# Performance work log

Measured on AMD Instinct MI355X. Metric: run time of the kernel, lower is better.

## Reference

```python
import jax, jax.numpy as jnp
import numpy as np

EPS = 1e-5

def layer_norm(x, w, b):
    m = jnp.mean(x, axis=-1, keepdims=True)
    v = jnp.mean(jnp.square(x - m), axis=-1, keepdims=True)
    return (x - m) * jax.lax.rsqrt(v + EPS) * w + b

def time_shift(x):
    # shift sequence right by one, zero-pad first step: (B,L,D)
    return jnp.pad(x[:, :-1], ((0, 0), (1, 0), (0, 0)))

def wkv(time_decay, time_first, k, v):
    # Numerically-stable RWKV v4 WKV recurrence. k,v: (B,L,D)
    w = -jnp.exp(time_decay)  # (D,) negative decay
    u = time_first            # (D,)
    B, L, D = k.shape
    kT = jnp.swapaxes(k, 0, 1)  # (L,B,D)
    vT = jnp.swapaxes(v, 0, 1)
    a0 = jnp.zeros((B, D), k.dtype)
    b0 = jnp.zeros((B, D), k.dtype)
    p0 = jnp.full((B, D), -1e38, k.dtype)

    def step(carry, kv_t):
        a, b, p = carry
        k_t, v_t = kv_t
        ww = u + k_t
        q = jnp.maximum(p, ww)
        e1 = jnp.exp(p - q)
        e2 = jnp.exp(ww - q)
        out = (e1 * a + e2 * v_t) / (e1 * b + e2)
        ww2 = p + w
        q2 = jnp.maximum(ww2, k_t)
        e1b = jnp.exp(ww2 - q2)
        e2b = jnp.exp(k_t - q2)
        return (e1b * a + e2b * v_t, e1b * b + e2b, q2), out

    _, outs = jax.lax.scan(step, (a0, b0, p0), (kT, vT))
    return jnp.swapaxes(outs, 0, 1)  # (B,L,D)

def setup_inputs() -> dict:
    key = jax.random.key(0)
    B, L, D, D_att, D_ffn = 8, 2048, 1024, 1024, 4096
    ks = jax.random.split(key, 16)
    s = 1.0 / np.sqrt(D)
    inp = {
        "x": jax.random.normal(ks[0], (B, L, D), jnp.float32),
        "ln_att_w": jnp.ones((D,), jnp.float32),
        "ln_att_b": jnp.zeros((D,), jnp.float32),
        "ln_ffn_w": jnp.ones((D,), jnp.float32),
        "ln_ffn_b": jnp.zeros((D,), jnp.float32),
        "att_time_decay": jax.random.normal(ks[1], (D_att,), jnp.float32) * 0.5,
        "att_time_first": jax.random.normal(ks[2], (D_att,), jnp.float32) * 0.5,
        "att_mix_k": jax.random.uniform(ks[3], (D,), jnp.float32),
        "att_mix_v": jax.random.uniform(ks[4], (D,), jnp.float32),
        "att_mix_r": jax.random.uniform(ks[5], (D,), jnp.float32),
        "att_Wk": jax.random.normal(ks[6], (D_att, D), jnp.float32) * s,
        "att_Wv": jax.random.normal(ks[7], (D_att, D), jnp.float32) * s,
        "att_Wr": jax.random.normal(ks[8], (D_att, D), jnp.float32) * s,
        "att_Wo": jax.random.normal(ks[9], (D, D_att), jnp.float32) * s,
        "ffn_mix_k": jax.random.uniform(ks[10], (D,), jnp.float32),
        "ffn_mix_r": jax.random.uniform(ks[11], (D,), jnp.float32),
        "ffn_Wk": jax.random.normal(ks[12], (D_ffn, D), jnp.float32) * s,
        "ffn_Wv": jax.random.normal(ks[13], (D, D_ffn), jnp.float32) * (1.0 / np.sqrt(D_ffn)),
        "ffn_Wr": jax.random.normal(ks[14], (D, D), jnp.float32) * s,
    }
    return inp

def rwkv_block(x, ln_att_w, ln_att_b, ln_ffn_w, ln_ffn_b,
               att_time_decay, att_time_first, att_mix_k, att_mix_v, att_mix_r,
               att_Wk, att_Wv, att_Wr, att_Wo,
               ffn_mix_k, ffn_mix_r, ffn_Wk, ffn_Wv, ffn_Wr):
    # --- time-mix (WKV attention) ---
    xa = layer_norm(x, ln_att_w, ln_att_b)
    xs = time_shift(xa)
    k = jnp.einsum('bld,ad->bla', xa * att_mix_k + xs * (1.0 - att_mix_k), att_Wk)
    v = jnp.einsum('bld,ad->bla', xa * att_mix_v + xs * (1.0 - att_mix_v), att_Wv)
    r = jnp.einsum('bld,ad->bla', xa * att_mix_r + xs * (1.0 - att_mix_r), att_Wr)
    att = jnp.einsum('bla,da->bld', jax.nn.sigmoid(r) * wkv(att_time_decay, att_time_first, k, v), att_Wo)
    x = x + att
    # --- channel-mix FFN ---
    xf = layer_norm(x, ln_ffn_w, ln_ffn_b)
    xs = time_shift(xf)
    kx = xf * ffn_mix_k + xs * (1.0 - ffn_mix_k)
    rx = xf * ffn_mix_r + xs * (1.0 - ffn_mix_r)
    h = jnp.square(jax.nn.relu(jnp.einsum('bld,fd->blf', kx, ffn_Wk)))
    ffn = jax.nn.sigmoid(jnp.einsum('bld,ed->ble', rx, ffn_Wr)) * jnp.einsum('blf,df->bld', h, ffn_Wv)
    return x + ffn

def reference(x, ln_att_w, ln_att_b, ln_ffn_w, ln_ffn_b,
              att_time_decay, att_time_first, att_mix_k, att_mix_v, att_mix_r,
              att_Wk, att_Wv, att_Wr, att_Wo,
              ffn_mix_k, ffn_mix_r, ffn_Wk, ffn_Wv, ffn_Wr):
    return rwkv_block(x, ln_att_w, ln_att_b, ln_ffn_w, ln_ffn_b,
                      att_time_decay, att_time_first, att_mix_k, att_mix_v, att_mix_r,
                      att_Wk, att_Wv, att_Wr, att_Wo,
                      ffn_mix_k, ffn_mix_r, ffn_Wk, ffn_Wv, ffn_Wr)
```

## Files before the change

### kernel.cpp

```cpp
#include <hip/hip_runtime.h>
#include <stdint.h>

#define DDIM 1024
#define LSEQ 2048
#define BSZ  8
#define FDIM 4096
#define MROWS (BSZ*LSEQ)
#define NCHUNK 32
#define CLEN  (LSEQ/NCHUNK)

typedef float        f32x4  __attribute__((ext_vector_type(4)));
typedef unsigned int u32x4  __attribute__((ext_vector_type(4)));

using gas_void = const __attribute__((address_space(1))) void;
using las_void = __attribute__((address_space(3))) void;

__device__ __forceinline__ void gload16(const void* g, void* l) {
    __builtin_amdgcn_global_load_lds((gas_void*)g, (las_void*)l, 16, 0, 0);
}

__device__ __forceinline__ void mfma_bf16(f32x4& d, u32x4 a, u32x4 b) {
    asm("v_mfma_f32_16x16x32_bf16 %0, %1, %2, %0" : "+v"(d) : "v"(a), "v"(b));
}

__device__ __forceinline__ unsigned short f2bf(float f) {
    __bf16 h = (__bf16)f;
    return __builtin_bit_cast(unsigned short, h);
}

__global__ __launch_bounds__(256) void cvt_bf16(const float* __restrict__ src,
                                                __bf16* __restrict__ dst, int n4)
{
    int i = blockIdx.x * 256 + threadIdx.x;
    if (i >= n4) return;
    float4 f = ((const float4*)src)[i];
    ushort4 o;
    o.x = f2bf(f.x); o.y = f2bf(f.y); o.z = f2bf(f.z); o.w = f2bf(f.w);
    ((ushort4*)dst)[i] = o;
}

__device__ __forceinline__ void blk_reduce4(float& a, float& b, float& c, float& d) {
#pragma unroll
    for (int off = 32; off >= 1; off >>= 1) {
        a += __shfl_xor(a, off, 64);
        b += __shfl_xor(b, off, 64);
        c += __shfl_xor(c, off, 64);
        d += __shfl_xor(d, off, 64);
    }
    __shared__ float sm[4][4];
    const int tid = threadIdx.x;
    if ((tid & 63) == 0) {
        sm[tid >> 6][0] = a; sm[tid >> 6][1] = b;
        sm[tid >> 6][2] = c; sm[tid >> 6][3] = d;
    }
    __syncthreads();
    a = sm[0][0] + sm[1][0] + sm[2][0] + sm[3][0];
    b = sm[0][1] + sm[1][1] + sm[2][1] + sm[3][1];
    c = sm[0][2] + sm[1][2] + sm[2][2] + sm[3][2];
    d = sm[0][3] + sm[1][3] + sm[2][3] + sm[3][3];
}

__global__ __launch_bounds__(256) void ln_mix3(
    const float* __restrict__ xin, const float* __restrict__ lnw, const float* __restrict__ lnb,
    const float* __restrict__ mkv, const float* __restrict__ mvv, const float* __restrict__ mrv,
    __bf16* __restrict__ ok, __bf16* __restrict__ ov, __bf16* __restrict__ orr)
{
    const int row = blockIdx.x;
    const int l   = row & (LSEQ - 1);
    const int tid = threadIdx.x;
    const size_t rbase = (size_t)row * DDIM;
    const float4 cur = ((const float4*)(xin + rbase))[tid];
    float4 prv = make_float4(0.f, 0.f, 0.f, 0.f);
    if (l > 0) prv = ((const float4*)(xin + rbase - DDIM))[tid];
    float s0 = cur.x + cur.y + cur.z + cur.w;
    float q0 = cur.x*cur.x + cur.y*cur.y + cur.z*cur.z + cur.w*cur.w;
    float s1 = prv.x + prv.y + prv.z + prv.w;
    float q1 = prv.x*prv.x + prv.y*prv.y + prv.z*prv.z + prv.w*prv.w;
    blk_reduce4(s0, q0, s1, q1);
    const float inv = 1.f / (float)DDIM;
    const float m0 = s0 * inv, m1 = s1 * inv;
    const float r0 = rsqrtf(fmaxf(q0 * inv - m0*m0, 0.f) + 1e-5f);
    const float r1 = rsqrtf(fmaxf(q1 * inv - m1*m1, 0.f) + 1e-5f);
    const float4 w4 = ((const float4*)lnw)[tid];
    const float4 b4 = ((const float4*)lnb)[tid];
    const float4 k4 = ((const float4*)mkv)[tid];
    const float4 v4 = ((const float4*)mvv)[tid];
    const float4 r4 = ((const float4*)mrv)[tid];
    const float cA[4] = {cur.x, cur.y, cur.z, cur.w};
    const float pA[4] = {prv.x, prv.y, prv.z, prv.w};
    const float wA[4] = {w4.x, w4.y, w4.z, w4.w};
    const float bA[4] = {b4.x, b4.y, b4.z, b4.w};
    const float kA[4] = {k4.x, k4.y, k4.z, k4.w};
    const float vA[4] = {v4.x, v4.y, v4.z, v4.w};
    const float rA[4] = {r4.x, r4.y, r4.z, r4.w};
    ushort4 pk, pv, pr;
    unsigned short* pkp = &pk.x; unsigned short* pvp = &pv.x; unsigned short* prp = &pr.x;
#pragma unroll
    for (int j = 0; j < 4; ++j) {
        float xa = (cA[j] - m0) * r0 * wA[j] + bA[j];
        float xs = (l > 0) ? ((pA[j] - m1) * r1 * wA[j] + bA[j]) : 0.f;
        pkp[j] = f2bf(xa * kA[j] + xs * (1.f - kA[j]));
        pvp[j] = f2bf(xa * vA[j] + xs * (1.f - vA[j]));
        prp[j] = f2bf(xa * rA[j] + xs * (1.f - rA[j]));
    }
    const size_t oi = (size_t)row * (DDIM/4) + tid;
    ((ushort4*)ok)[oi]  = pk;
    ((ushort4*)ov)[oi]  = pv;
    ((ushort4*)orr)[oi] = pr;
}

__global__ __launch_bounds__(256) void ln_mix2(
    const float* __restrict__ xin, const float* __restrict__ lnw, const float* __restrict__ lnb,
    const float* __restrict__ mkv, const float* __restrict__ mrv,
    __bf16* __restrict__ ok, __bf16* __restrict__ orr)
{
    const int row = blockIdx.x;
    const int l   = row & (LSEQ - 1);
    const int tid = threadIdx.x;
    const size_t rbase = (size_t)row * DDIM;
    const float4 cur = ((const float4*)(xin + rbase))[tid];
    float4 prv = make_float4(0.f, 0.f, 0.f, 0.f);
    if (l > 0) prv = ((const float4*)(xin + rbase - DDIM))[tid];
    float s0 = cur.x + cur.y + cur.z + cur.w;
    float q0 = cur.x*cur.x + cur.y*cur.y + cur.z*cur.z + cur.w*cur.w;
    float s1 = prv.x + prv.y + prv.z + prv.w;
    float q1 = prv.x*prv.x + prv.y*prv.y + prv.z*prv.z + prv.w*prv.w;
    blk_reduce4(s0, q0, s1, q1);
    const float inv = 1.f / (float)DDIM;
    const float m0 = s0 * inv, m1 = s1 * inv;
    const float r0 = rsqrtf(fmaxf(q0 * inv - m0*m0, 0.f) + 1e-5f);
    const float r1 = rsqrtf(fmaxf(q1 * inv - m1*m1, 0.f) + 1e-5f);
    const float4 w4 = ((const float4*)lnw)[tid];
    const float4 b4 = ((const float4*)lnb)[tid];
    const float4 k4 = ((const float4*)mkv)[tid];
    const float4 r4 = ((const float4*)mrv)[tid];
    const float cA[4] = {cur.x, cur.y, cur.z, cur.w};
    const float pA[4] = {prv.x, prv.y, prv.z, prv.w};
    const float wA[4] = {w4.x, w4.y, w4.z, w4.w};
    const float bA[4] = {b4.x, b4.y, b4.z, b4.w};
    const float kA[4] = {k4.x, k4.y, k4.z, k4.w};
    const float rA[4] = {r4.x, r4.y, r4.z, r4.w};
    ushort4 pk, pr;
    unsigned short* pkp = &pk.x; unsigned short* prp = &pr.x;
#pragma unroll
    for (int j = 0; j < 4; ++j) {
        float xa = (cA[j] - m0) * r0 * wA[j] + bA[j];
        float xs = (l > 0) ? ((pA[j] - m1) * r1 * wA[j] + bA[j]) : 0.f;
        pkp[j] = f2bf(xa * kA[j] + xs * (1.f - kA[j]));
        prp[j] = f2bf(xa * rA[j] + xs * (1.f - rA[j]));
    }
    const size_t oi = (size_t)row * (DDIM/4) + tid;
    ((ushort4*)ok)[oi]  = pk;
    ((ushort4*)orr)[oi] = pr;
}


__global__ __launch_bounds__(256) void wkv_phase1(
    const __bf16* __restrict__ kin, const __bf16* __restrict__ vin,
    const float* __restrict__ td,
    float* __restrict__ sa, float* __restrict__ sb, float* __restrict__ sp)
{
    const int idx = blockIdx.x * 256 + threadIdx.x;
    const int d  = idx & (DDIM - 1);
    const int bc = idx >> 10;
    const int b  = bc & (BSZ - 1);
    const int c  = bc >> 3;
    const float w = -__expf(td[d]);
    const size_t base = ((size_t)b * LSEQ + (size_t)c * CLEN) * DDIM + d;
    float a = 0.f, bbv = 0.f, p = -1e38f;
    for (int t = 0; t < CLEN; ++t) {
        const size_t off = base + (size_t)t * DDIM;
        const float kt = (float)kin[off];
        const float vt = (float)vin[off];
        const float ww2 = p + w;
        const float q2  = fmaxf(ww2, kt);
        const float e1  = __expf(ww2 - q2);
        const float e2  = __expf(kt - q2);
        a   = e1 * a   + e2 * vt;
        bbv = e1 * bbv + e2;
        p   = q2;
    }
    sa[idx] = a; sb[idx] = bbv; sp[idx] = p;
}

__global__ __launch_bounds__(256) void wkv_phase2(
    const __bf16* __restrict__ kin, const __bf16* __restrict__ vin,
    const __bf16* __restrict__ srin,
    const float* __restrict__ td, const float* __restrict__ tf,
    const float* __restrict__ sa, const float* __restrict__ sb,
    const float* __restrict__ sp,
    __bf16* __restrict__ outp)
{
    const int idx = blockIdx.x * 256 + threadIdx.x;
    const int d  = idx & (DDIM - 1);
    const int bc = idx >> 10;
    const int b  = bc & (BSZ - 1);
    const int c  = bc >> 3;
    const float w = -__expf(td[d]);
    const float u = tf[d];
    const float nw = (float)CLEN * w;

    float a = 0.f, bbv = 0.f, p = -1e38f;
    for (int j = 0; j < c; ++j) {
        const int sidx = ((j * BSZ + b) << 10) + d;
        const float aj = sa[sidx], bj = sb[sidx], pj = sp[sidx];
        const float ps = p + nw;
        const float pn = fmaxf(ps, pj);
        const float e1 = __expf(ps - pn);
        const float e2 = __expf(pj - pn);
        a   = e1 * a   + e2 * aj;
        bbv = e1 * bbv + e2 * bj;
        p   = pn;
    }

    const size_t base = ((size_t)b * LSEQ + (size_t)c * CLEN) * DDIM + d;
    for (int t = 0; t < CLEN; ++t) {
        const size_t off = base + (size_t)t * DDIM;
        const float kt = (float)kin[off];
        const float vt = (float)vin[off];
        const float sr = (float)srin[off];
        const float ww = u + kt;
        const float q  = fmaxf(p, ww);
        const float e1 = __expf(p - q);
        const float e2 = __expf(ww - q);
        const float o  = (e1 * a + e2 * vt) / (e1 * bbv + e2);
        outp[off] = (__bf16)(sr * o);
        const float ww2 = p + w;
        const float q2  = fmaxf(ww2, kt);
        const float e1b = __expf(ww2 - q2);
        const float e2b = __expf(kt - q2);
        a   = e1b * a   + e2b * vt;
        bbv = e1b * bbv + e2b;
        p   = q2;
    }
}

template<int EPI>
__global__ __launch_bounds__(256)
void gemm_bt(const __bf16* __restrict__ A, const __bf16* __restrict__ Bw,
             float* outF, __bf16* outH,
             const float* auxF, const __bf16* __restrict__ auxH,
             int N, int K)
{
    __shared__ __bf16 As[128 * 32];
    __shared__ __bf16 Bs[128 * 32];
    const int tid  = threadIdx.x;
    const int lane = tid & 63;
    const int wid  = tid >> 6;
    const int wr = wid >> 1, wc = wid & 1;
    const size_t row0 = (size_t)blockIdx.x * 128;
    const size_t col0 = (size_t)blockIdx.y * 128;

    const int c0 = wid * 2, c1 = c0 + 1;
    const int srow = lane >> 2;
    const int scol = (lane & 3) << 3;
    const __bf16* aG0 = A  + (row0 + c0 * 16 + srow) * (size_t)K + scol;
    const __bf16* aG1 = A  + (row0 + c1 * 16 + srow) * (size_t)K + scol;
    const __bf16* bG0 = Bw + (col0 + c0 * 16 + srow) * (size_t)K + scol;
    const __bf16* bG1 = Bw + (col0 + c1 * 16 + srow) * (size_t)K + scol;
    __bf16* aL0 = &As[c0 * 512];
    __bf16* aL1 = &As[c1 * 512];
    __bf16* bL0 = &Bs[c0 * 512];
    __bf16* bL1 = &Bs[c1 * 512];

    f32x4 acc[4][4] = {};

    const int aoff = (wr * 64 + (lane & 15)) * 32 + ((lane >> 4) << 3);
    const int boff = (wc * 64 + (lane & 15)) * 32 + ((lane >> 4) << 3);

    for (int k0 = 0; k0 < K; k0 += 32) {
        __syncthreads();
        gload16(aG0 + k0, aL0);
        gload16(aG1 + k0, aL1);
        gload16(bG0 + k0, bL0);
        gload16(bG1 + k0, bL1);
        __syncthreads();
        u32x4 af[4], bf[4];
#pragma unroll
        for (int m = 0; m < 4; ++m) af[m] = *(const u32x4*)&As[aoff + m * 512];
#pragma unroll
        for (int n = 0; n < 4; ++n) bf[n] = *(const u32x4*)&Bs[boff + n * 512];
#pragma unroll
        for (int m = 0; m < 4; ++m)
#pragma unroll
            for (int n = 0; n < 4; ++n)
                mfma_bf16(acc[m][n], af[m], bf[n]);
    }
    asm volatile("s_nop 7\n\ts_nop 7\n\ts_nop 3");

    const size_t obr = row0 + wr * 64 + ((lane >> 4) << 2);
    const size_t obc = col0 + wc * 64 + (lane & 15);
#pragma unroll
    for (int m = 0; m < 4; ++m) {
#pragma unroll
        for (int n = 0; n < 4; ++n) {
#pragma unroll
            for (int j = 0; j < 4; ++j) {
                const size_t idx = (obr + m * 16 + j) * (size_t)N + obc + n * 16;
                const float v = acc[m][n][j];
                if constexpr (EPI == 1) {
                    outH[idx] = (__bf16)(1.f / (1.f + __expf(-v)));
                } else if constexpr (EPI == 2) {
                    const float t = fmaxf(v, 0.f);
                    outH[idx] = (__bf16)(t * t);
                } else if constexpr (EPI == 3) {
                    outF[idx] = auxF[idx] + v;
                } else if constexpr (EPI == 4) {
                    outF[idx] = auxF[idx] + (float)auxH[idx] * v;
                } else {
                    outH[idx] = (__bf16)v;
                }
            }
        }
    }
}

extern "C" void kernel_launch(void* const* d_in, const int* in_sizes, int n_in,
                              void* d_out, int out_size, void* d_ws, size_t ws_size,
                              hipStream_t stream)
{
    const float* x    = (const float*)d_in[0];
    const float* lnaw = (const float*)d_in[1];
    const float* lnab = (const float*)d_in[2];
    const float* lnfw = (const float*)d_in[3];
    const float* lnfb = (const float*)d_in[4];
    const float* tdec = (const float*)d_in[5];
    const float* tfir = (const float*)d_in[6];
    const float* amk  = (const float*)d_in[7];
    const float* amv  = (const float*)d_in[8];
    const float* amr  = (const float*)d_in[9];
    const float* aWk  = (const float*)d_in[10];
    const float* aWv  = (const float*)d_in[11];
    const float* aWr  = (const float*)d_in[12];
    const float* aWo  = (const float*)d_in[13];
    const float* fmk  = (const float*)d_in[14];
    const float* fmr  = (const float*)d_in[15];
    const float* fWk  = (const float*)d_in[16];
    const float* fWv  = (const float*)d_in[17];
    const float* fWr  = (const float*)d_in[18];
    float* out = (float*)d_out;

    char* ws = (char*)d_ws;
    const size_t MiB = 1ull << 20;
    __bf16* Wk_h  = (__bf16*)ws;
    __bf16* Wv_h  = Wk_h + (1ull << 20);
    __bf16* Wr_h  = Wk_h + (2ull << 20);
    __bf16* Wo_h  = Wk_h + (3ull << 20);
    __bf16* fWk_h = Wk_h + (4ull << 20);
    __bf16* fWv_h = Wk_h + (8ull << 20);
    __bf16* fWr_h = Wk_h + (12ull << 20);
    __bf16* xk = (__bf16*)(ws + 26 * MiB);
    __bf16* xv = (__bf16*)(ws + 58 * MiB);
    __bf16* xr = (__bf16*)(ws + 90 * MiB);
    __bf16* kb = (__bf16*)(ws + 122 * MiB);
    __bf16* vb = (__bf16*)(ws + 154 * MiB);
    __bf16* sr = (__bf16*)(ws + 186 * MiB);
    float* st_a = (float*)(ws + 218 * MiB);
    float* st_b = (float*)(ws + 219 * MiB);
    float* st_p = (float*)(ws + 220 * MiB);
    __bf16* atta = xk;
    __bf16* kx   = xv;
    __bf16* rx   = xr;
    __bf16* sb   = xk;
    __bf16* hb   = (__bf16*)(ws + 90 * MiB);

    cvt_bf16<<<1024, 256, 0, stream>>>(aWk, Wk_h,  1 << 18);
    cvt_bf16<<<1024, 256, 0, stream>>>(aWv, Wv_h,  1 << 18);
    cvt_bf16<<<1024, 256, 0, stream>>>(aWr, Wr_h,  1 << 18);
    cvt_bf16<<<1024, 256, 0, stream>>>(aWo, Wo_h,  1 << 18);
    cvt_bf16<<<4096, 256, 0, stream>>>(fWk, fWk_h, 1 << 20);
    cvt_bf16<<<4096, 256, 0, stream>>>(fWv, fWv_h, 1 << 20);
    cvt_bf16<<<1024, 256, 0, stream>>>(fWr, fWr_h, 1 << 18);

    ln_mix3<<<MROWS, 256, 0, stream>>>(x, lnaw, lnab, amk, amv, amr, xk, xv, xr);

    dim3 blk(256);
    dim3 gD(MROWS / 128, DDIM / 128);
    gemm_bt<5><<<gD, blk, 0, stream>>>(xk, Wk_h, nullptr, kb, nullptr, nullptr, DDIM, DDIM);
    gemm_bt<5><<<gD, blk, 0, stream>>>(xv, Wv_h, nullptr, vb, nullptr, nullptr, DDIM, DDIM);
    gemm_bt<1><<<gD, blk, 0, stream>>>(xr, Wr_h, nullptr, sr, nullptr, nullptr, DDIM, DDIM);

    const int nthreads = BSZ * DDIM * NCHUNK;
    wkv_phase1<<<nthreads / 256, 256, 0, stream>>>(kb, vb, tdec, st_a, st_b, st_p);
    wkv_phase2<<<nthreads / 256, 256, 0, stream>>>(kb, vb, sr, tdec, tfir,
                                                   st_a, st_b, st_p, atta);

    gemm_bt<3><<<gD, blk, 0, stream>>>(atta, Wo_h, out, nullptr, x, nullptr, DDIM, DDIM);

    ln_mix2<<<MROWS, 256, 0, stream>>>(out, lnfw, lnfb, fmk, fmr, kx, rx);

    gemm_bt<1><<<gD, blk, 0, stream>>>(rx, fWr_h, nullptr, sb, nullptr, nullptr, DDIM, DDIM);

    dim3 gF(MROWS / 128, FDIM / 128);
    gemm_bt<2><<<gF, blk, 0, stream>>>(kx, fWk_h, nullptr, hb, nullptr, nullptr, FDIM, DDIM);

    gemm_bt<4><<<gD, blk, 0, stream>>>(hb, fWv_h, out, nullptr, out, sb, DDIM, FDIM);
}
```

Measured before the change: 796.3 us.

## Replace GEMM with 256x256-tile, 8-wave, multi-buffered swizzled-LDS kernel

Replaces the 128x128 single-buffered bf16 MFMA GEMM with a 256x256-tile kernel using 512 threads, a 4-deep LDS ring with XOR-swizzled layout, and prefetch two k-steps ahead using vmcnt waits. Adds an XCD-aware block remapping and s_setprio around MFMA bursts. The aim is more data reuse per tile, fewer LDS bank conflicts, and hiding global load latency behind compute. In exchange it uses 128 KB of shared memory and many accumulator registers, which may limit occupancy.

```diff
diff --git a/kernel.cpp b/kernel.cpp
--- a/kernel.cpp
+++ b/kernel.cpp
@@ -154,7 +154,6 @@
     ((ushort4*)orr)[oi] = pr;
 }
 
-
 __global__ __launch_bounds__(256) void wkv_phase1(
     const __bf16* __restrict__ kin, const __bf16* __restrict__ vin,
     const float* __restrict__ td,
@@ -236,62 +235,94 @@
 }
 
 template<int EPI>
-__global__ __launch_bounds__(256)
-void gemm_bt(const __bf16* __restrict__ A, const __bf16* __restrict__ Bw,
-             float* outF, __bf16* outH,
-             const float* auxF, const __bf16* __restrict__ auxH,
-             int N, int K)
-{
-    __shared__ __bf16 As[128 * 32];
-    __shared__ __bf16 Bs[128 * 32];
+__global__ __launch_bounds__(512, 2)
+void gemm8(const __bf16* __restrict__ A, const __bf16* __restrict__ Bw,
+           float* outF, __bf16* outH,
+           const float* auxF, const __bf16* __restrict__ auxH,
+           int N, int K, int gy)
+{
+    __shared__ __align__(16) char smem[131072];
     const int tid  = threadIdx.x;
     const int lane = tid & 63;
     const int wid  = tid >> 6;
-    const int wr = wid >> 1, wc = wid & 1;
-    const size_t row0 = (size_t)blockIdx.x * 128;
-    const size_t col0 = (size_t)blockIdx.y * 128;
-
-    const int c0 = wid * 2, c1 = c0 + 1;
-    const int srow = lane >> 2;
-    const int scol = (lane & 3) << 3;
-    const __bf16* aG0 = A  + (row0 + c0 * 16 + srow) * (size_t)K + scol;
-    const __bf16* aG1 = A  + (row0 + c1 * 16 + srow) * (size_t)K + scol;
-    const __bf16* bG0 = Bw + (col0 + c0 * 16 + srow) * (size_t)K + scol;
-    const __bf16* bG1 = Bw + (col0 + c1 * 16 + srow) * (size_t)K + scol;
-    __bf16* aL0 = &As[c0 * 512];
-    __bf16* aL1 = &As[c1 * 512];
-    __bf16* bL0 = &Bs[c0 * 512];
-    __bf16* bL1 = &Bs[c1 * 512];
-
-    f32x4 acc[4][4] = {};
-
-    const int aoff = (wr * 64 + (lane & 15)) * 32 + ((lane >> 4) << 3);
-    const int boff = (wc * 64 + (lane & 15)) * 32 + ((lane >> 4) << 3);
-
-    for (int k0 = 0; k0 < K; k0 += 32) {
-        __syncthreads();
-        gload16(aG0 + k0, aL0);
-        gload16(aG1 + k0, aL1);
-        gload16(bG0 + k0, bL0);
-        gload16(bG1 + k0, bL1);
-        __syncthreads();
-        u32x4 af[4], bf[4];
-#pragma unroll
-        for (int m = 0; m < 4; ++m) af[m] = *(const u32x4*)&As[aoff + m * 512];
-#pragma unroll
-        for (int n = 0; n < 4; ++n) bf[n] = *(const u32x4*)&Bs[boff + n * 512];
+    const int wr = wid >> 2, wc = wid & 3;
+
+    const int nwg = gridDim.x;
+    const int f = blockIdx.x;
+    const int g = (f & 7) * (nwg >> 3) + (f >> 3);
+    const int tx = g / gy;
+    const int ty = g - tx * gy;
+    const size_t row0 = (size_t)tx * 256;
+    const size_t col0 = (size_t)ty * 256;
+
+    auto stage = [&](int buf, int k0, int isB, int q) {
+        const int row  = q * 128 + (tid >> 2);
+        const int slot = (tid & 3) ^ ((row >> 1) & 3);
+        const __bf16* gp = (isB ? Bw + (col0 + row) * (size_t)K
+                                : A  + (row0 + row) * (size_t)K) + k0 + slot * 8;
+        char* lp = smem + buf * 32768 + isB * 16384 + q * 8192 + wid * 1024;
+        gload16(gp, lp);
+    };
+    auto rdA = [&](int buf, int m) -> u32x4 {
+        const int row  = wr * 128 + m * 16 + (lane & 15);
+        const int slot = (lane >> 4) ^ ((row >> 1) & 3);
+        return *(const u32x4*)(smem + buf * 32768 + row * 64 + slot * 16);
+    };
+    auto rdB = [&](int buf, int n) -> u32x4 {
+        const int row  = wc * 64 + n * 16 + (lane & 15);
+        const int slot = (lane >> 4) ^ ((row >> 1) & 3);
+        return *(const u32x4*)(smem + buf * 32768 + 16384 + row * 64 + slot * 16);
+    };
+
+    f32x4 acc[8][4] = {};
+    const int ns = K / 32;
+
+    stage(0, 0, 0, 0); stage(0, 0, 0, 1); stage(0, 0, 1, 0); stage(0, 0, 1, 1);
+    stage(1, 32, 0, 0); stage(1, 32, 0, 1); stage(1, 32, 1, 0); stage(1, 32, 1, 1);
+
+    for (int t = 0; t < ns; ++t) {
+        const int cb = t & 3;
+        if (t < ns - 1) asm volatile("s_waitcnt vmcnt(4)" ::: "memory");
+        else            asm volatile("s_waitcnt vmcnt(0)" ::: "memory");
+        __builtin_amdgcn_s_barrier();
+
+        const int pf = t + 2;
+        const int pb = pf & 3;
+        const int pk = pf * 32;
+
+        u32x4 bfr[4];
+#pragma unroll
+        for (int n = 0; n < 4; ++n) bfr[n] = rdB(cb, n);
+        u32x4 afr[4];
+#pragma unroll
+        for (int m = 0; m < 4; ++m) afr[m] = rdA(cb, m);
+        if (pf < ns) { stage(pb, pk, 0, 0); stage(pb, pk, 0, 1); }
+        __builtin_amdgcn_s_setprio(1);
 #pragma unroll
         for (int m = 0; m < 4; ++m)
 #pragma unroll
             for (int n = 0; n < 4; ++n)
-                mfma_bf16(acc[m][n], af[m], bf[n]);
+                mfma_bf16(acc[m][n], afr[m], bfr[n]);
+        __builtin_amdgcn_s_setprio(0);
+        __builtin_amdgcn_s_barrier();
+
+#pragma unroll
+        for (int m = 0; m < 4; ++m) afr[m] = rdA(cb, m + 4);
+        if (pf < ns) { stage(pb, pk, 1, 0); stage(pb, pk, 1, 1); }
+        __builtin_amdgcn_s_setprio(1);
+#pragma unroll
+        for (int m = 0; m < 4; ++m)
+#pragma unroll
+            for (int n = 0; n < 4; ++n)
+                mfma_bf16(acc[m + 4][n], afr[m], bfr[n]);
+        __builtin_amdgcn_s_setprio(0);
     }
     asm volatile("s_nop 7\n\ts_nop 7\n\ts_nop 3");
 
-    const size_t obr = row0 + wr * 64 + ((lane >> 4) << 2);
+    const size_t obr = row0 + wr * 128 + ((lane >> 4) << 2);
     const size_t obc = col0 + wc * 64 + (lane & 15);
 #pragma unroll
-    for (int m = 0; m < 4; ++m) {
+    for (int m = 0; m < 8; ++m) {
 #pragma unroll
         for (int n = 0; n < 4; ++n) {
 #pragma unroll
@@ -301,8 +332,8 @@
                 if constexpr (EPI == 1) {
                     outH[idx] = (__bf16)(1.f / (1.f + __expf(-v)));
                 } else if constexpr (EPI == 2) {
-                    const float t = fmaxf(v, 0.f);
-                    outH[idx] = (__bf16)(t * t);
+                    const float t2 = fmaxf(v, 0.f);
+                    outH[idx] = (__bf16)(t2 * t2);
                 } else if constexpr (EPI == 3) {
                     outF[idx] = auxF[idx] + v;
                 } else if constexpr (EPI == 4) {
@@ -374,25 +405,24 @@
 
     ln_mix3<<<MROWS, 256, 0, stream>>>(x, lnaw, lnab, amk, amv, amr, xk, xv, xr);
 
-    dim3 blk(256);
-    dim3 gD(MROWS / 128, DDIM / 128);
-    gemm_bt<5><<<gD, blk, 0, stream>>>(xk, Wk_h, nullptr, kb, nullptr, nullptr, DDIM, DDIM);
-    gemm_bt<5><<<gD, blk, 0, stream>>>(xv, Wv_h, nullptr, vb, nullptr, nullptr, DDIM, DDIM);
-    gemm_bt<1><<<gD, blk, 0, stream>>>(xr, Wr_h, nullptr, sr, nullptr, nullptr, DDIM, DDIM);
+    const int gD = (MROWS / 256) * (DDIM / 256);
+    const int gF = (MROWS / 256) * (FDIM / 256);
+    gemm8<5><<<gD, 512, 0, stream>>>(xk, Wk_h, nullptr, kb, nullptr, nullptr, DDIM, DDIM, DDIM/256);
+    gemm8<5><<<gD, 512, 0, stream>>>(xv, Wv_h, nullptr, vb, nullptr, nullptr, DDIM, DDIM, DDIM/256);
+    gemm8<1><<<gD, 512, 0, stream>>>(xr, Wr_h, nullptr, sr, nullptr, nullptr, DDIM, DDIM, DDIM/256);
 
     const int nthreads = BSZ * DDIM * NCHUNK;
     wkv_phase1<<<nthreads / 256, 256, 0, stream>>>(kb, vb, tdec, st_a, st_b, st_p);
     wkv_phase2<<<nthreads / 256, 256, 0, stream>>>(kb, vb, sr, tdec, tfir,
                                                    st_a, st_b, st_p, atta);
 
-    gemm_bt<3><<<gD, blk, 0, stream>>>(atta, Wo_h, out, nullptr, x, nullptr, DDIM, DDIM);
+    gemm8<3><<<gD, 512, 0, stream>>>(atta, Wo_h, out, nullptr, x, nullptr, DDIM, DDIM, DDIM/256);
 
     ln_mix2<<<MROWS, 256, 0, stream>>>(out, lnfw, lnfb, fmk, fmr, kx, rx);
 
-    gemm_bt<1><<<gD, blk, 0, stream>>>(rx, fWr_h, nullptr, sb, nullptr, nullptr, DDIM, DDIM);
-
-    dim3 gF(MROWS / 128, FDIM / 128);
-    gemm_bt<2><<<gF, blk, 0, stream>>>(kx, fWk_h, nullptr, hb, nullptr, nullptr, FDIM, DDIM);
-
-    gemm_bt<4><<<gD, blk, 0, stream>>>(hb, fWv_h, out, nullptr, out, sb, DDIM, FDIM);
-}
+    gemm8<1><<<gD, 512, 0, stream>>>(rx, fWr_h, nullptr, sb, nullptr, nullptr, DDIM, DDIM, DDIM/256);
+
+    gemm8<2><<<gF, 512, 0, stream>>>(kx, fWk_h, nullptr, hb, nullptr, nullptr, FDIM, DDIM, FDIM/256);
+
+    gemm8<4><<<gD, 512, 0, stream>>>(hb, fWv_h, out, nullptr, out, sb, DDIM, FDIM, DDIM/256);
+}
```

Result: faster. 737.4 us (-7.4%).
